# Optimization experiments

Hardware: AMD Instinct MI355X
Metric: run time of the kernel (lower is better)

## Reference

```python
import jax, jax.numpy as jnp
import numpy as np

B, N, D, H = 8, 1024, 1024, 16
DH = D // H
REL_VOCAB = 6  # stadia + 2
NEG_INF = -1e9


def setup_inputs() -> dict:
    key = jax.random.key(0)
    ks = jax.random.split(key, 8)
    hid = jax.random.normal(ks[0], (B, N, D), dtype=jnp.float32)
    adj = jax.random.randint(ks[1], (B, N, N), 0, 2, dtype=jnp.int32)
    relative_pos = jax.random.randint(ks[2], (B, N, N), 0, REL_VOCAB, dtype=jnp.int32)
    s = 1.0 / np.sqrt(D)
    Wq = jax.random.normal(ks[3], (D, D), dtype=jnp.float32) * s
    Wk = jax.random.normal(ks[4], (D, D), dtype=jnp.float32) * s
    Wv = jax.random.normal(ks[5], (D, D), dtype=jnp.float32) * s
    rel_table = jax.random.normal(ks[6], (REL_VOCAB, 1), dtype=jnp.float32)
    ln_gamma = jnp.ones((D,), dtype=jnp.float32)
    ln_beta = jnp.zeros((D,), dtype=jnp.float32)
    return {"hid": hid, "adj": adj, "relative_pos": relative_pos,
            "Wq": Wq, "Wk": Wk, "Wv": Wv, "rel_table": rel_table,
            "ln_gamma": ln_gamma, "ln_beta": ln_beta}


def _layer_norm(x, gamma, beta, eps=1e-5):
    mu = jnp.mean(x, axis=-1, keepdims=True)
    var = jnp.var(x, axis=-1, keepdims=True)
    return (x - mu) * jax.lax.rsqrt(var + eps) * gamma + beta


def reference(hid, adj, relative_pos, Wq, Wk, Wv, rel_table, ln_gamma, ln_beta):
    # relative position bias: embedding dim 1, squeezed -> [B, N, N]
    rel_bias = rel_table[relative_pos][..., 0]
    # projections, split into heads: [B, N, H, DH]
    q = (hid @ Wq).reshape(B, N, H, DH)
    k = (hid @ Wk).reshape(B, N, H, DH)
    v = (hid @ Wv).reshape(B, N, H, DH)
    # scores [B, H, N, N], scaled by sqrt(key_dim) = sqrt(D)
    scores = jnp.einsum('bqhd,bkhd->bhqk', q, k) / jnp.sqrt(jnp.float32(D))
    scores = scores + rel_bias[:, None, :, :]
    mask = (adj != 0)[:, None, :, :]
    scores = jnp.where(mask, scores, NEG_INF)
    attn = jax.nn.softmax(scores, axis=-1)
    out = jnp.einsum('bhqk,bkhd->bqhd', attn, v).reshape(B, N, D)
    out = jax.nn.relu(out) + hid  # activation + residual
    return _layer_norm(out, ln_gamma, ln_beta)
```

## Files before the change

### kernel.cpp

```cpp
#include <hip/hip_runtime.h>
#include <math.h>

#define Bc 8
#define Nc 1024
#define Dc 1024
#define Hc 16
#define DHc 64
#define NEGINF -1e9f

typedef unsigned int  u32;
typedef unsigned short u16;
typedef unsigned long long u64;
typedef u16  u16x8 __attribute__((ext_vector_type(8)));
typedef u16  u16x4 __attribute__((ext_vector_type(4)));
typedef __bf16 bf16x8 __attribute__((ext_vector_type(8)));
typedef float f32x4 __attribute__((ext_vector_type(4)));

__device__ __forceinline__ u16 f2bf(float f) {
    u32 u = __builtin_bit_cast(u32, f);
    u += 0x7fffu + ((u >> 16) & 1u);
    return (u16)(u >> 16);
}
__device__ __forceinline__ float bf2f(u16 b) {
    return __builtin_bit_cast(float, (u32)b << 16);
}
__device__ __forceinline__ u32 pack2bf(float lo, float hi) {
    return __builtin_amdgcn_perm(__builtin_bit_cast(u32, hi),
                                 __builtin_bit_cast(u32, lo), 0x07060302u);
}

__device__ __forceinline__ void glds16(const u16* g, const u16* l) {
    __builtin_amdgcn_global_load_lds(
        (const __attribute__((address_space(1))) void*)(u64)g,
        (__attribute__((address_space(3))) void*)(u32)(u64)l, 16, 0, 0);
}

__global__ __launch_bounds__(256) void bias_prep(
    const int* __restrict__ adj, const int* __restrict__ relpos,
    const float* __restrict__ rel_table, u16* __restrict__ bias)
{
    __shared__ float tbl[8];
    int t = threadIdx.x;
    if (t < 6) tbl[t] = rel_table[t];
    __syncthreads();
    int idx = blockIdx.x * 256 + t;
    int4 a  = ((const int4*)adj)[idx];
    int4 rp = ((const int4*)relpos)[idx];
    u16x4 o;
    o.x = a.x ? f2bf(tbl[rp.x]) : f2bf(NEGINF);
    o.y = a.y ? f2bf(tbl[rp.y]) : f2bf(NEGINF);
    o.z = a.z ? f2bf(tbl[rp.z]) : f2bf(NEGINF);
    o.w = a.w ? f2bf(tbl[rp.w]) : f2bf(NEGINF);
    ((u16x4*)bias)[idx] = o;
}

__global__ __launch_bounds__(256) void hid2bf(const float* __restrict__ in,
                                              u16* __restrict__ out)
{
    int idx = blockIdx.x * 256 + threadIdx.x;
    float4 a = ((const float4*)in)[2 * idx];
    float4 b = ((const float4*)in)[2 * idx + 1];
    u16x8 o;
    o[0] = f2bf(a.x); o[1] = f2bf(a.y); o[2] = f2bf(a.z); o[3] = f2bf(a.w);
    o[4] = f2bf(b.x); o[5] = f2bf(b.y); o[6] = f2bf(b.z); o[7] = f2bf(b.w);
    ((u16x8*)out)[idx] = o;
}

__global__ __launch_bounds__(256) void wtrans(
    const float* __restrict__ Wq, const float* __restrict__ Wk,
    const float* __restrict__ Wv, u16* __restrict__ WqT,
    u16* __restrict__ WkT, u16* __restrict__ WvT)
{
    const float* W; u16* WT;
    if (blockIdx.z == 0)      { W = Wq; WT = WqT; }
    else if (blockIdx.z == 1) { W = Wk; WT = WkT; }
    else                      { W = Wv; WT = WvT; }
    __shared__ float tile[32][33];
    int tx = threadIdx.x, ty = threadIdx.y;
    int n0 = blockIdx.x * 32, k0 = blockIdx.y * 32;
#pragma unroll
    for (int i = 0; i < 4; ++i) {
        int r = ty + i * 8;
        tile[r][tx] = W[(size_t)(k0 + r) * Dc + n0 + tx];
    }
    __syncthreads();
#pragma unroll
    for (int i = 0; i < 4; ++i) {
        int n = ty + i * 8;
        WT[(size_t)(n0 + n) * Dc + k0 + tx] = f2bf(tile[tx][n]);
    }
}

__global__ __launch_bounds__(256) void qkv_mfma(
    const u16* __restrict__ hidb, const u16* __restrict__ WqT,
    const u16* __restrict__ WkT, const u16* __restrict__ WvT,
    u16* __restrict__ qo, u16* __restrict__ ko, u16* __restrict__ vo)
{
    __shared__ u16 As[128 * 64];
    __shared__ u16 Bs[128 * 64];

    const int bx = blockIdx.x, by = blockIdx.y;
    const int z = bx >> 3;
    const int c0 = (bx << 7) & 1023;
    const int row0 = by << 7;
    const u16* WT; u16* out;
    if (z == 0)      { WT = WqT; out = qo; }
    else if (z == 1) { WT = WkT; out = ko; }
    else             { WT = WvT; out = vo; }

    const int tid = threadIdx.x;
    const int wave = tid >> 6, lane = tid & 63;
    const int g = lane >> 4, li = lane & 15;
    const int wr = wave >> 1, wc = wave & 1;
    const int lr = lane >> 3, ls = lane & 7;
    const int sseg = ls ^ lr;

    const u16* pa = hidb + (size_t)(row0 + wave * 32 + lr) * Dc + sseg * 8;
    const u16* pb = WT   + (size_t)(c0   + wave * 32 + lr) * Dc + sseg * 8;
    u16* la = &As[(wave * 32) * 64];
    u16* lb = &Bs[(wave * 32) * 64];

    f32x4 acc[4][4] = {};

    const int swz = (li & 7);

    for (int kt = 0; kt < Dc; kt += 64) {
        __syncthreads();
#pragma unroll
        for (int i = 0; i < 4; ++i) {
            glds16(pa + kt + i * 8 * Dc, la + i * 8 * 64);
            glds16(pb + kt + i * 8 * Dc, lb + i * 8 * 64);
        }
        __syncthreads();
#pragma unroll
        for (int ks = 0; ks < 2; ++ks) {
            const int soff = ((ks * 4 + g) ^ swz) * 8;
            bf16x8 af[4], bf[4];
#pragma unroll
            for (int mi = 0; mi < 4; ++mi)
                af[mi] = *(const bf16x8*)&As[(wr * 64 + mi * 16 + li) * 64 + soff];
#pragma unroll
            for (int nj = 0; nj < 4; ++nj)
                bf[nj] = *(const bf16x8*)&Bs[(wc * 64 + nj * 16 + li) * 64 + soff];
#pragma unroll
            for (int mi = 0; mi < 4; ++mi)
#pragma unroll
                for (int nj = 0; nj < 4; ++nj)
                    acc[mi][nj] = __builtin_amdgcn_mfma_f32_16x16x32_bf16(
                        af[mi], bf[nj], acc[mi][nj], 0, 0, 0);
        }
    }

    const int b = row0 >> 10;

    if (z != 2) {
        const int nbase = (row0 & 1023) + wr * 64 + g * 4;
#pragma unroll
        for (int mi = 0; mi < 4; ++mi)
#pragma unroll
            for (int rr = 0; rr < 4; ++rr) {
                int n = nbase + mi * 16 + rr;
#pragma unroll
                for (int nj = 0; nj < 4; ++nj) {
                    int cz = c0 + wc * 64 + nj * 16 + li;
                    out[(((size_t)(b * Hc + (cz >> 6)) * Nc + n) * DHc) + (cz & 63)]
                        = f2bf(acc[mi][nj][rr]);
                }
            }
    } else {
        __syncthreads();
        u16* T = ((wave & 2) ? Bs : As) + (wave & 1) * 4096;
#pragma unroll
        for (int mi = 0; mi < 4; ++mi)
#pragma unroll
            for (int rr = 0; rr < 4; ++rr) {
                int r = mi * 16 + g * 4 + rr;
                int pp = ((r & 15) << 2) | (r >> 4);
#pragma unroll
                for (int nj = 0; nj < 4; ++nj) {
                    int c = nj * 16 + li;
                    T[c * 64 + ((((pp >> 3) ^ (c & 7)) << 3) | (pp & 7))]
                        = f2bf(acc[mi][nj][rr]);
                }
            }
        const int nseg = ls ^ lr;
#pragma unroll
        for (int i = 0; i < 8; ++i) {
            int cl = i * 8 + lr;
            u16x8 val = *(const u16x8*)&T[cl * 64 + ls * 8];
            int cz = c0 + wc * 64 + cl;
            int n = (row0 & 1023) + wr * 64 + nseg * 8;
            *(u16x8*)&out[(((size_t)(b * Hc + (cz >> 6)) * DHc + (cz & 63)) * Nc) + n] = val;
        }
    }
}

__global__ __launch_bounds__(256, 4) void attn_mfma(
    const u16* __restrict__ q, const u16* __restrict__ k,
    const u16* __restrict__ v, const u16* __restrict__ bias,
    float* __restrict__ attn_out)
{
    __shared__ u16 Ks[64 * 64];
    __shared__ u16 VTs[64 * 64];
    __shared__ u16 PQ[128 * 72];

    const int tid = threadIdx.x;
    const int w = tid >> 6, lane = tid & 63;
    const int g = lane >> 4, li = lane & 15;
    const int lr8 = lane >> 3, ls8 = lane & 7;
    const int lseg = ls8 ^ lr8;

    const int id = blockIdx.x;
    const int p  = (id & 7) | ((id >> 6) << 3);
    const int qt = (id >> 3) & 7;
    const int b = p >> 4, h = p & 15;
    const int q0 = qt << 7;

    {
        const int sr = tid >> 1;
        const int sh = (tid & 1) * 32;
        const u16* qp = q + ((size_t)((b * Hc + h) * Nc) + q0 + sr) * DHc + sh;
        u16x8 a0 = *(const u16x8*)qp;
        u16x8 a1 = *(const u16x8*)(qp + 8);
        u16x8 a2 = *(const u16x8*)(qp + 16);
        u16x8 a3 = *(const u16x8*)(qp + 24);
        u16* dst = &PQ[sr * 72 + sh];
        *(u16x8*)(dst)      = a0; *(u16x8*)(dst + 8)  = a1;
        *(u16x8*)(dst + 16) = a2; *(u16x8*)(dst + 24) = a3;
    }
    __syncthreads();

    bf16x8 qf[2][2];
#pragma unroll
    for (int mt = 0; mt < 2; ++mt)
#pragma unroll
        for (int ks = 0; ks < 2; ++ks)
            qf[mt][ks] = *(const bf16x8*)&PQ[(w * 32 + mt * 16 + li) * 72 + ks * 32 + g * 8];

    f32x4 o_[2][4] = {};
    float lsum[2][4] = {};

    const float scale = 0.03125f;
    const u16* kbase = k + (size_t)(b * Hc + h) * Nc * DHc;
    const u16* vbase = v + (size_t)(b * Hc + h) * DHc * Nc;
    const u16* brow  = bias + ((size_t)(b * Nc) + q0 + w * 32) * Nc + li;

    for (int k0 = 0; k0 < Nc; k0 += 64) {
        __syncthreads();
        {
            const u16* kp = kbase + (size_t)(k0 + w * 16 + lr8) * DHc + lseg * 8;
            const u16* vp = vbase + (size_t)(w * 16 + lr8) * Nc + k0 + lseg * 8;
            u16* kl = &Ks[(w * 16) * 64];
            u16* vl = &VTs[(w * 16) * 64];
            glds16(kp,           kl);
            glds16(kp + 8 * DHc, kl + 8 * 64);
            glds16(vp,           vl);
            glds16(vp + 8 * Nc,  vl + 8 * 64);
        }
        __syncthreads();

        f32x4 sacc[2][4] = {};
#pragma unroll
        for (int ks = 0; ks < 2; ++ks) {
            const int so = (((ks << 2) | g) ^ (li & 7)) << 3;
#pragma unroll
            for (int nt = 0; nt < 4; ++nt) {
                bf16x8 kf = *(const bf16x8*)&Ks[(nt * 16 + li) * 64 + so];
                sacc[0][nt] = __builtin_amdgcn_mfma_f32_16x16x32_bf16(qf[0][ks], kf, sacc[0][nt], 0, 0, 0);
                sacc[1][nt] = __builtin_amdgcn_mfma_f32_16x16x32_bf16(qf[1][ks], kf, sacc[1][nt], 0, 0, 0);
            }
        }

#pragma unroll
        for (int mt = 0; mt < 2; ++mt)
#pragma unroll
            for (int r = 0; r < 4; ++r) {
                const int qrl = mt * 16 + g * 4 + r;
                const u16* bp = brow + (size_t)qrl * Nc + k0;
                float pv[4];
#pragma unroll
                for (int nt = 0; nt < 4; ++nt) {
                    float sv = sacc[mt][nt][r] * scale + bf2f(bp[nt * 16]);
                    pv[nt] = __expf(sv);
                    lsum[mt][r] += pv[nt];
                }
                u32* dst = (u32*)&PQ[(w * 32 + qrl) * 72 + li * 4];
                dst[0] = pack2bf(pv[0], pv[1]);
                dst[1] = pack2bf(pv[2], pv[3]);
            }

#pragma unroll
        for (int ks = 0; ks < 2; ++ks) {
            const int so = (((ks << 2) | g) ^ (li & 7)) << 3;
            bf16x8 pa0 = *(const bf16x8*)&PQ[(w * 32 + li) * 72 + ks * 32 + g * 8];
            bf16x8 pa1 = *(const bf16x8*)&PQ[(w * 32 + 16 + li) * 72 + ks * 32 + g * 8];
#pragma unroll
            for (int j = 0; j < 4; ++j) {
                bf16x8 vf = *(const bf16x8*)&VTs[(j * 16 + li) * 64 + so];
                o_[0][j] = __builtin_amdgcn_mfma_f32_16x16x32_bf16(pa0, vf, o_[0][j], 0, 0, 0);
                o_[1][j] = __builtin_amdgcn_mfma_f32_16x16x32_bf16(pa1, vf, o_[1][j], 0, 0, 0);
            }
        }
    }

#pragma unroll
    for (int mt = 0; mt < 2; ++mt)
#pragma unroll
        for (int r = 0; r < 4; ++r) {
            float l = lsum[mt][r];
            l += __shfl_xor(l, 1);
            l += __shfl_xor(l, 2);
            l += __shfl_xor(l, 4);
            l += __shfl_xor(l, 8);
            float inv = 1.f / l;
            int qrow = q0 + w * 32 + mt * 16 + g * 4 + r;
            float* op = attn_out + ((size_t)b * Nc + qrow) * Dc + h * DHc;
#pragma unroll
            for (int j = 0; j < 4; ++j)
                op[j * 16 + li] = o_[mt][j][r] * inv;
        }
}

__global__ __launch_bounds__(256) void ln_kernel(
    const float* attn_out, const float* __restrict__ hid,
    const float* __restrict__ gamma, const float* __restrict__ beta,
    float* out)
{
    const int row = blockIdx.x;
    const int t = threadIdx.x;

    float4 av = *(const float4*)&attn_out[(size_t)row * Dc + t * 4];
    float4 hv = *(const float4*)&hid[(size_t)row * Dc + t * 4];
    float x0 = fmaxf(av.x, 0.f) + hv.x;
    float x1 = fmaxf(av.y, 0.f) + hv.y;
    float x2 = fmaxf(av.z, 0.f) + hv.z;
    float x3 = fmaxf(av.w, 0.f) + hv.w;

    float s1 = x0 + x1 + x2 + x3;
    float s2 = x0 * x0 + x1 * x1 + x2 * x2 + x3 * x3;
#pragma unroll
    for (int off = 1; off < 64; off <<= 1) {
        s1 += __shfl_xor(s1, off);
        s2 += __shfl_xor(s2, off);
    }
    __shared__ float w1[4], w2[4];
    int lane = t & 63, wid = t >> 6;
    if (lane == 0) { w1[wid] = s1; w2[wid] = s2; }
    __syncthreads();
    s1 = w1[0] + w1[1] + w1[2] + w1[3];
    s2 = w2[0] + w2[1] + w2[2] + w2[3];

    float mu  = s1 * (1.f / 1024.f);
    float var = s2 * (1.f / 1024.f) - mu * mu;
    float rstd = rsqrtf(var + 1e-5f);

    float4 g  = *(const float4*)&gamma[t * 4];
    float4 be = *(const float4*)&beta[t * 4];
    float4 r4;
    r4.x = (x0 - mu) * rstd * g.x + be.x;
    r4.y = (x1 - mu) * rstd * g.y + be.y;
    r4.z = (x2 - mu) * rstd * g.z + be.z;
    r4.w = (x3 - mu) * rstd * g.w + be.w;
    *(float4*)&out[(size_t)row * Dc + t * 4] = r4;
}

extern "C" void kernel_launch(void* const* d_in, const int* in_sizes, int n_in,
                              void* d_out, int out_size, void* d_ws, size_t ws_size,
                              hipStream_t stream) {
    const float* hid       = (const float*)d_in[0];
    const int*   adj       = (const int*)d_in[1];
    const int*   relpos    = (const int*)d_in[2];
    const float* Wq        = (const float*)d_in[3];
    const float* Wk        = (const float*)d_in[4];
    const float* Wv        = (const float*)d_in[5];
    const float* rel_table = (const float*)d_in[6];
    const float* gamma     = (const float*)d_in[7];
    const float* beta      = (const float*)d_in[8];
    float* out = (float*)d_out;

    const size_t per  = (size_t)Bc * Hc * Nc * DHc;
    const size_t wsz  = (size_t)Dc * Dc;
    u16* qb   = (u16*)d_ws;
    u16* kb   = qb + per;
    u16* vb   = kb + per;
    u16* bias = vb + per;
    u16* hidb = bias + (size_t)Bc * Nc * Nc;
    u16* wqT  = hidb + (size_t)Bc * Nc * Dc;
    u16* wkT  = wqT + wsz;
    u16* wvT  = wkT + wsz;

    bias_prep<<<(Bc * Nc * Nc) / (4 * 256), 256, 0, stream>>>(adj, relpos, rel_table, bias);
    hid2bf<<<(Bc * Nc * Dc) / (8 * 256), 256, 0, stream>>>(hid, hidb);
    wtrans<<<dim3(32, 32, 3), dim3(32, 8), 0, stream>>>(Wq, Wk, Wv, wqT, wkT, wvT);
    qkv_mfma<<<dim3(24, 64), 256, 0, stream>>>(hidb, wqT, wkT, wvT, qb, kb, vb);
    attn_mfma<<<1024, 256, 0, stream>>>(qb, kb, vb, bias, out);
    ln_kernel<<<Bc * Nc, 256, 0, stream>>>(out, hid, gamma, beta, out);
}
```

Before: 338.2 us.

## Permute bias layout so attention loads four bias values per lane in one vector

The bias prep kernel now writes the bias in a permuted order within each 64-column block, so the four values a lane needs (columns li, li+16, li+32, li+48) sit next to each other. The attention kernel then fetches them as one 8-byte vector load per row and issues those loads before the barrier, overlapping them with the K/V copy into shared memory. This replaces four scattered 2-byte loads per row. In exchange, the prep kernel reads adj and relpos with strided scalar loads instead of int4 vector loads, and more registers are held across the barrier.

```diff
diff --git a/kernel.cpp b/kernel.cpp
--- a/kernel.cpp
+++ b/kernel.cpp
@@ -43,15 +43,21 @@
     int t = threadIdx.x;
     if (t < 6) tbl[t] = rel_table[t];
     __syncthreads();
-    int idx = blockIdx.x * 256 + t;
-    int4 a  = ((const int4*)adj)[idx];
-    int4 rp = ((const int4*)relpos)[idx];
+    int i = blockIdx.x * 256 + t;
+    int pos4 = i << 2;
+    int row  = pos4 >> 10;
+    int p    = pos4 & 1023;
+    int blk  = p & ~63;
+    int m    = (p & 63) >> 2;
+    size_t base = ((size_t)row << 10) + blk + m;
     u16x4 o;
-    o.x = a.x ? f2bf(tbl[rp.x]) : f2bf(NEGINF);
-    o.y = a.y ? f2bf(tbl[rp.y]) : f2bf(NEGINF);
-    o.z = a.z ? f2bf(tbl[rp.z]) : f2bf(NEGINF);
-    o.w = a.w ? f2bf(tbl[rp.w]) : f2bf(NEGINF);
-    ((u16x4*)bias)[idx] = o;
+#pragma unroll
+    for (int j = 0; j < 4; ++j) {
+        int a  = adj[base + 16 * j];
+        int rp = relpos[base + 16 * j];
+        o[j] = a ? f2bf(tbl[rp]) : f2bf(NEGINF);
+    }
+    ((u16x4*)bias)[i] = o;
 }
 
 __global__ __launch_bounds__(256) void hid2bf(const float* __restrict__ in,
@@ -243,7 +249,7 @@
     const float scale = 0.03125f;
     const u16* kbase = k + (size_t)(b * Hc + h) * Nc * DHc;
     const u16* vbase = v + (size_t)(b * Hc + h) * DHc * Nc;
-    const u16* brow  = bias + ((size_t)(b * Nc) + q0 + w * 32) * Nc + li;
+    const u16* brow  = bias + ((size_t)(b * Nc) + q0 + w * 32) * Nc + 4 * li;
 
     for (int k0 = 0; k0 < Nc; k0 += 64) {
         __syncthreads();
@@ -257,6 +263,12 @@
             glds16(vp,           vl);
             glds16(vp + 8 * Nc,  vl + 8 * 64);
         }
+        u16x4 brv[2][4];
+#pragma unroll
+        for (int mt = 0; mt < 2; ++mt)
+#pragma unroll
+            for (int r = 0; r < 4; ++r)
+                brv[mt][r] = *(const u16x4*)&brow[(size_t)(mt * 16 + g * 4 + r) * Nc + k0];
         __syncthreads();
 
         f32x4 sacc[2][4] = {};
@@ -276,11 +288,10 @@
 #pragma unroll
             for (int r = 0; r < 4; ++r) {
                 const int qrl = mt * 16 + g * 4 + r;
-                const u16* bp = brow + (size_t)qrl * Nc + k0;
                 float pv[4];
 #pragma unroll
                 for (int nt = 0; nt < 4; ++nt) {
-                    float sv = sacc[mt][nt][r] * scale + bf2f(bp[nt * 16]);
+                    float sv = sacc[mt][nt][r] * scale + bf2f(brv[mt][r][nt]);
                     pv[nt] = __expf(sv);
                     lsum[mt][r] += pv[nt];
                 }
```

Result: faster. 298.3 us (-11.8%).
